# Performance work log

Hardware: AMD Instinct MI355X
Metric: run time of the kernel (lower is better)

## Reference

```python
import jax, jax.numpy as jnp
import numpy as np


def setup_inputs() -> dict:
    key = jax.random.key(0)
    k1, k2 = jax.random.split(key)
    B, D, H, W = 4, 64, 64, 64
    M = 4096
    z = jax.random.normal(k1, (B, D, H, W), dtype=jnp.float32)
    e = jax.random.normal(k2, (M, D), dtype=jnp.float32)
    log_sigma = jnp.zeros((1,), dtype=jnp.float32)
    return {"z": z, "e": e, "log_sigma": log_sigma}


def reference(z, e, log_sigma):
    # z: [B, D, H, W] latents, e: [M, D] codebook, log_sigma: [1] parameter
    T = 1.0  # latent_temp default
    B, D, H, W = z.shape
    zf = jnp.transpose(z, (0, 2, 3, 1)).reshape(-1, D)  # [N, D]
    N = zf.shape[0]
    # squared pairwise distances via ||z||^2 + ||e||^2 - 2 z e^T (avoids [N,M,D] intermediate)
    d2 = (jnp.sum(zf * zf, axis=1)[:, None]
          + jnp.sum(e * e, axis=1)[None, :]
          - 2.0 * zf @ e.T)  # [N, M]
    alpha = -1.0 / (2.0 * jnp.exp(log_sigma[0]) ** 2)
    matrix = alpha * d2 / T  # [N, M]
    lse = jax.nn.logsumexp(matrix, axis=0)  # [M], reduce over N points per code
    # np.log(np.e) == 1.0
    loss = (-jnp.mean(T * lse)
            + 0.5 * D * (2.0 * log_sigma[0] - 1.0)
            + jnp.log(jnp.asarray(N, dtype=jnp.float32)))
    return loss
```

## Files before the change

kernel.cpp:

```cpp
#include <hip/hip_runtime.h>
#include <hip/hip_bf16.h>
#include <math.h>

#define D_   64
#define HW_  4096
#define N_   16384
#define M_   4096

#define BM 128
#define NSPLIT 32
#define NCHUNK (N_ / NSPLIT)
#define NTILES (NCHUNK / 128)

#define AZN_OFF 0
#define AEN_OFF 16384
#define SUM_OFF 20480
#define ZTB_OFF 24576
#define EBF_OFF (24576 + 524288)
#define FAST_WS_FLOATS (EBF_OFF + 131072)

#define FB_AZN 0
#define FB_AEN N_
#define FB_PART (N_ + M_)

#define L2E 1.4426950408889634f

typedef __attribute__((ext_vector_type(8))) short short8;
typedef __attribute__((ext_vector_type(16))) float floatx16;

#if __has_builtin(__builtin_amdgcn_exp2f)
#define EXP2F(x) __builtin_amdgcn_exp2f(x)
#else
#define EXP2F(x) exp2f(x)
#endif

__device__ __forceinline__ unsigned int bf16_rne(float x) {
    unsigned int u = __float_as_uint(x);
    u += 0x7fffu + ((u >> 16) & 1u);
    return u >> 16;
}


__global__ void prep_kernel(const float* __restrict__ z,
                            const float* __restrict__ e,
                            const float* __restrict__ lsp,
                            float* __restrict__ ws) {
    const float ls = lsp[0];
    const float alpha = -0.5f * __expf(-2.f * ls);
    const float anl = alpha * L2E;
    const float c2p = -2.f * alpha * L2E;
    unsigned short* zTb = (unsigned short*)(ws + ZTB_OFF);
    unsigned short* ebf = (unsigned short*)(ws + EBF_OFF);
    const int blk = blockIdx.x, t = threadIdx.x;

    if (blk < 256) {
        __shared__ float lt[64 * 65];
        const int b = blk >> 6, hw0 = (blk & 63) * 64;
        const int n0 = b * HW_ + hw0;
        const float* zb = z + ((size_t)b * D_) * HW_ + hw0;
#pragma unroll
        for (int i = 0; i < 4; ++i) {
            int idx = t + 256 * i;
            int d = idx >> 4, c = (idx & 15) * 4;
            float4 v = *(const float4*)(zb + (size_t)d * HW_ + c);
            float* p = &lt[d * 65 + c];
            p[0] = v.x; p[1] = v.y; p[2] = v.z; p[3] = v.w;
        }
        __syncthreads();
#pragma unroll
        for (int j = 0; j < 2; ++j) {
            int idx = t + 256 * j;
            int nl = idx >> 3, g = idx & 7;
            float v[8]; float s = 0.f;
#pragma unroll
            for (int jj = 0; jj < 8; ++jj) {
                v[jj] = lt[(8 * g + jj) * 65 + nl];
                s = fmaf(v[jj], v[jj], s);
            }
            s += __shfl_xor(s, 1);
            s += __shfl_xor(s, 2);
            s += __shfl_xor(s, 4);
            uint4 pk;
            pk.x = bf16_rne(v[0] * c2p) | (bf16_rne(v[1] * c2p) << 16);
            pk.y = bf16_rne(v[2] * c2p) | (bf16_rne(v[3] * c2p) << 16);
            pk.z = bf16_rne(v[4] * c2p) | (bf16_rne(v[5] * c2p) << 16);
            pk.w = bf16_rne(v[6] * c2p) | (bf16_rne(v[7] * c2p) << 16);
            *(uint4*)(zTb + (size_t)(n0 + nl) * 64 + 8 * g) = pk;
            if (g == 0) ws[AZN_OFF + n0 + nl] = anl * s;
        }
    } else {
        int m = (blk - 256) * 256 + t;
        const float4* ep = (const float4*)(e + (size_t)m * D_);
        float s = 0.f;
        unsigned int pk[32];
#pragma unroll
        for (int k = 0; k < 16; ++k) {
            float4 v = ep[k];
            s += v.x * v.x + v.y * v.y + v.z * v.z + v.w * v.w;
            pk[2 * k]     = bf16_rne(v.x) | (bf16_rne(v.y) << 16);
            pk[2 * k + 1] = bf16_rne(v.z) | (bf16_rne(v.w) << 16);
        }
        uint4* op = (uint4*)(ebf + (size_t)m * 64);
#pragma unroll
        for (int k = 0; k < 8; ++k)
            op[k] = make_uint4(pk[4 * k], pk[4 * k + 1], pk[4 * k + 2], pk[4 * k + 3]);
        ws[AEN_OFF + m] = anl * s;
        ws[SUM_OFF + m] = 0.f;
    }
}

__global__ __launch_bounds__(256, 2) void main_fast(float* __restrict__ ws) {
    __shared__ float lds_red[BM];
    const unsigned short* zTb = (const unsigned short*)(ws + ZTB_OFF);
    const unsigned short* ebf = (const unsigned short*)(ws + EBF_OFF);
    const float* azn = ws + AZN_OFF;
    const float* aen = ws + AEN_OFF;
    float* sums = ws + SUM_OFF;

    const int m0 = blockIdx.x * BM;
    const int ns = blockIdx.y;
    const int t = threadIdx.x;
    const int lane = t & 63;
    const int w = t >> 6;
    const int rlo = lane & 31;
    const int kh = lane >> 5;

    short8 bf[4][4];
    float aen_r[4];
#pragma unroll
    for (int mt = 0; mt < 4; ++mt) {
        int row = m0 + mt * 32 + rlo;
        aen_r[mt] = aen[row];
#pragma unroll
        for (int ks = 0; ks < 4; ++ks)
            bf[mt][ks] = *(const short8*)(ebf + (size_t)row * 64 + (ks * 2 + kh) * 8);
    }

    float sum[4] = {0.f, 0.f, 0.f, 0.f};
    const int nbase = ns * NCHUNK + w * 32;

#pragma unroll
    for (int tile = 0; tile < NTILES; ++tile) {
        const int nr = nbase + tile * 128;
        short8 af[4];
#pragma unroll
        for (int ks = 0; ks < 4; ++ks)
            af[ks] = *(const short8*)(zTb + (size_t)(nr + rlo) * 64 + (ks * 2 + kh) * 8);

        float azn_r[16];
        const int r0 = nr + 4 * kh;
#pragma unroll
        for (int rg = 0; rg < 4; ++rg) {
            float4 vv = *(const float4*)(azn + r0 + 8 * rg);
            azn_r[rg * 4 + 0] = vv.x; azn_r[rg * 4 + 1] = vv.y;
            azn_r[rg * 4 + 2] = vv.z; azn_r[rg * 4 + 3] = vv.w;
        }

        floatx16 acc[4];
#pragma unroll
        for (int mt = 0; mt < 4; ++mt)
#pragma unroll
            for (int r = 0; r < 16; ++r)
                acc[mt][r] = azn_r[r] + aen_r[mt];

#pragma unroll
        for (int ks = 0; ks < 4; ++ks)
#pragma unroll
            for (int mt = 0; mt < 4; ++mt)
                acc[mt] = __builtin_amdgcn_mfma_f32_32x32x16_bf16(
                    af[ks], bf[mt][ks], acc[mt], 0, 0, 0);

#pragma unroll
        for (int mt = 0; mt < 4; ++mt) {
            float s = 0.f;
#pragma unroll
            for (int r = 0; r < 16; ++r) s += EXP2F(acc[mt][r]);
            sum[mt] += s;
        }
    }

#pragma unroll
    for (int mt = 0; mt < 4; ++mt) sum[mt] += __shfl_down(sum[mt], 32);

    if (t < BM) lds_red[t] = 0.f;
    __syncthreads();
    if (lane < 32) {
#pragma unroll
        for (int mt = 0; mt < 4; ++mt) atomicAdd(&lds_red[mt * 32 + rlo], sum[mt]);
    }
    __syncthreads();
    if (t < BM) atomicAdd(&sums[m0 + t], lds_red[t]);
}

__global__ void finalize_fast(const float* __restrict__ ws,
                              const float* __restrict__ lsp,
                              float* __restrict__ out) {
    __shared__ double red[256];
    const float* sums = ws + SUM_OFF;
    int t = threadIdx.x;
    double local = 0.0;
#pragma unroll
    for (int j = 0; j < 16; ++j) {
        float s = sums[t + 256 * j];
        local += (double)logf(s);
    }
    red[t] = local;
    __syncthreads();
    for (int off = 128; off > 0; off >>= 1) {
        if (t < off) red[t] += red[t + off];
        __syncthreads();
    }
    if (t == 0) {
        double ls = (double)lsp[0];
        double loss = -(red[0] / (double)M_)
                      + 0.5 * (double)D_ * (2.0 * ls - 1.0)
                      + log((double)N_);
        out[0] = (float)loss;
    }
}


__global__ void norms_kernel(const float* __restrict__ z,
                             const float* __restrict__ e,
                             const float* __restrict__ lsp,
                             float* __restrict__ ws) {
    float ls = lsp[0];
    float alpha = -0.5f * __expf(-2.f * ls);
    int blk = blockIdx.x, t = threadIdx.x;
    if (blk < 64) {
        int n = blk * 256 + t;
        int b = n >> 12, hw = n & 4095;
        const float* zp = z + (size_t)b * D_ * HW_ + hw;
        float s = 0.f;
#pragma unroll
        for (int d = 0; d < D_; ++d) { float v = zp[(size_t)d * HW_]; s = fmaf(v, v, s); }
        ws[FB_AZN + n] = alpha * s;
    } else {
        int m = (blk - 64) * 256 + t;
        const float4* ep = (const float4*)(e + (size_t)m * D_);
        float s = 0.f;
#pragma unroll
        for (int k = 0; k < 16; ++k) {
            float4 v = ep[k];
            s += v.x * v.x + v.y * v.y + v.z * v.z + v.w * v.w;
        }
        ws[FB_AEN + m] = alpha * s;
    }
}

__global__ __launch_bounds__(256, 2) void main_lds(
        const float* __restrict__ z, const float* __restrict__ e,
        const float* __restrict__ lsp, const float* __restrict__ ws,
        float* __restrict__ partial) {
    __shared__ unsigned short lds_a[128 * 64];
    __shared__ unsigned short lds_b[BM * 64];
    __shared__ float lds_azn[128];
    __shared__ float lds_red[BM];

    const int m0 = blockIdx.x * BM;
    const int ns = blockIdx.y;
    const int t = threadIdx.x;
    const int lane = t & 63;
    const int w = t >> 6;
    const int rlo = lane & 31;
    const int kh = lane >> 5;

    const float ls = lsp[0];
    const float c2 = __expf(-2.f * ls);

    const float* azn_g = ws + FB_AZN;
    const float* aen_g = ws + FB_AEN;

#pragma unroll
    for (int i = 0; i < 8; ++i) {
        int idx = t + 256 * i;
        int m = idx >> 4, f4 = idx & 15;
        float4 v = *(const float4*)(e + (size_t)(m0 + m) * D_ + f4 * 4);
        unsigned int p0 = bf16_rne(v.x) | (bf16_rne(v.y) << 16);
        unsigned int p1 = bf16_rne(v.z) | (bf16_rne(v.w) << 16);
        int un = m * 8 + ((f4 >> 1) ^ (m & 7));
        unsigned int* dst = (unsigned int*)&lds_b[un * 8 + (f4 & 1) * 4];
        dst[0] = p0; dst[1] = p1;
    }
    float aen_r[4];
#pragma unroll
    for (int mt = 0; mt < 4; ++mt) aen_r[mt] = aen_g[m0 + mt * 32 + rlo];
    __syncthreads();

    short8 bfr[4][4];
#pragma unroll
    for (int mt = 0; mt < 4; ++mt)
#pragma unroll
        for (int ks = 0; ks < 4; ++ks) {
            int row = mt * 32 + rlo;
            int g = ks * 2 + kh;
            bfr[mt][ks] = *(const short8*)&lds_b[(row * 8 + (g ^ (row & 7))) * 8];
        }

    float sum[4] = {0.f, 0.f, 0.f, 0.f};

    for (int tile = 0; tile < NTILES; ++tile) {
        int n0 = ns * NCHUNK + tile * 128;
        int b   = n0 >> 12;
        int hw0 = n0 & 4095;
        __syncthreads();
#pragma unroll
        for (int i = 0; i < 4; ++i) {
            int idx = t + 256 * i;
            int dp = idx >> 5;
            int c4 = idx & 31;
            int d0 = dp * 2;
            const float* zp = z + ((size_t)(b * D_ + d0)) * HW_ + hw0 + c4 * 4;
            float4 v0 = *(const float4*)zp;
            float4 v1 = *(const float4*)(zp + HW_);
            int g = d0 >> 3;
            float a0[4] = {v0.x, v0.y, v0.z, v0.w};
            float a1[4] = {v1.x, v1.y, v1.z, v1.w};
#pragma unroll
            for (int q = 0; q < 4; ++q) {
                int row = c4 * 4 + q;
                unsigned int pk = bf16_rne(a0[q]) | (bf16_rne(a1[q]) << 16);
                int un = row * 8 + (g ^ (row & 7));
                *(unsigned int*)&lds_a[un * 8 + (d0 & 7)] = pk;
            }
        }
        if (t < 128) lds_azn[t] = azn_g[n0 + t];
        __syncthreads();

        short8 af[4];
        int arow = w * 32 + rlo;
#pragma unroll
        for (int ks = 0; ks < 4; ++ks) {
            int g = ks * 2 + kh;
            af[ks] = *(const short8*)&lds_a[(arow * 8 + (g ^ (arow & 7))) * 8];
        }
        float azn_r[16];
        int r0 = w * 32 + 4 * kh;
#pragma unroll
        for (int rg = 0; rg < 4; ++rg) {
            float4 vv = *(const float4*)&lds_azn[r0 + 8 * rg];
            azn_r[rg * 4 + 0] = vv.x; azn_r[rg * 4 + 1] = vv.y;
            azn_r[rg * 4 + 2] = vv.z; azn_r[rg * 4 + 3] = vv.w;
        }

        floatx16 acc[4] = {};
#pragma unroll
        for (int ks = 0; ks < 4; ++ks)
#pragma unroll
            for (int mt = 0; mt < 4; ++mt)
                acc[mt] = __builtin_amdgcn_mfma_f32_32x32x16_bf16(
                    af[ks], bfr[mt][ks], acc[mt], 0, 0, 0);

#pragma unroll
        for (int mt = 0; mt < 4; ++mt) {
            float s = 0.f;
#pragma unroll
            for (int r = 0; r < 16; ++r) {
                float val = fmaf(acc[mt][r], c2, azn_r[r]) + aen_r[mt];
                s += __expf(val);
            }
            sum[mt] += s;
        }
    }

#pragma unroll
    for (int mt = 0; mt < 4; ++mt) sum[mt] += __shfl_down(sum[mt], 32);

    __syncthreads();
    if (t < BM) lds_red[t] = 0.f;
    __syncthreads();
    if (lane < 32) {
#pragma unroll
        for (int mt = 0; mt < 4; ++mt) atomicAdd(&lds_red[mt * 32 + rlo], sum[mt]);
    }
    __syncthreads();
    if (t < BM) partial[(size_t)ns * M_ + m0 + t] = lds_red[t];
}

__global__ void finalize_part(const float* __restrict__ partial,
                              const float* __restrict__ lsp,
                              float* __restrict__ out) {
    __shared__ double red[256];
    int t = threadIdx.x;
    double local = 0.0;
#pragma unroll
    for (int j = 0; j < 16; ++j) {
        int m = t + 256 * j;
        float s = 0.f;
#pragma unroll
        for (int k = 0; k < NSPLIT; ++k) s += partial[(size_t)k * M_ + m];
        local += (double)logf(s);
    }
    red[t] = local;
    __syncthreads();
    for (int off = 128; off > 0; off >>= 1) {
        if (t < off) red[t] += red[t + off];
        __syncthreads();
    }
    if (t == 0) {
        double ls = (double)lsp[0];
        double loss = -(red[0] / (double)M_)
                      + 0.5 * (double)D_ * (2.0 * ls - 1.0)
                      + log((double)N_);
        out[0] = (float)loss;
    }
}

extern "C" void kernel_launch(void* const* d_in, const int* in_sizes, int n_in,
                              void* d_out, int out_size, void* d_ws, size_t ws_size,
                              hipStream_t stream) {
    const float* z   = (const float*)d_in[0];
    const float* e   = (const float*)d_in[1];
    const float* lsp = (const float*)d_in[2];
    float* ws  = (float*)d_ws;
    float* out = (float*)d_out;

    if (ws_size >= (size_t)FAST_WS_FLOATS * sizeof(float)) {
        hipLaunchKernelGGL(prep_kernel, dim3(272), dim3(256), 0, stream, z, e, lsp, ws);
        hipLaunchKernelGGL(main_fast, dim3(M_ / BM, NSPLIT), dim3(256), 0, stream, ws);
        hipLaunchKernelGGL(finalize_fast, dim3(1), dim3(256), 0, stream, ws, lsp, out);
    } else {
        hipLaunchKernelGGL(norms_kernel, dim3(80), dim3(256), 0, stream, z, e, lsp, ws);
        hipLaunchKernelGGL(main_lds, dim3(M_ / BM, NSPLIT), dim3(256), 0, stream,
                           z, e, lsp, ws, ws + FB_PART);
        hipLaunchKernelGGL(finalize_part, dim3(1), dim3(256), 0, stream,
                           ws + FB_PART, lsp, out);
    }
}
```

Measured before the change: 86.47 us.

## Shrink codebook tile, lengthen N chunks, and prefetch next z tile in registers

Each main_fast block now covers 64 codes instead of 128 and splits N into 16 chunks instead of 32, so every block runs 8 N-tiles rather than 4. The z fragment and its norms for the next tile are loaded into registers while the current tile computes, a software double buffer meant to hide global load latency. Occupancy is raised to 3 waves per SIMD. The grid stays at 1024 blocks but each block does half the MFMA work per tile and reloads z twice as often relative to compute. The fallback path is hardcoded to its old sizes so it keeps working.

New measurement: 91.41 us. 1.06x slower.

```diff
diff --git a/kernel.cpp b/kernel.cpp
--- a/kernel.cpp
+++ b/kernel.cpp
@@ -7,8 +7,8 @@
 #define N_   16384
 #define M_   4096
 
-#define BM 128
-#define NSPLIT 32
+#define BM 64
+#define NSPLIT 16
 #define NCHUNK (N_ / NSPLIT)
 #define NTILES (NCHUNK / 128)
 
@@ -109,7 +109,7 @@
     }
 }
 
-__global__ __launch_bounds__(256, 2) void main_fast(float* __restrict__ ws) {
+__global__ __launch_bounds__(256, 3) void main_fast(float* __restrict__ ws) {
     __shared__ float lds_red[BM];
     const unsigned short* zTb = (const unsigned short*)(ws + ZTB_OFF);
     const unsigned short* ebf = (const unsigned short*)(ws + EBF_OFF);
@@ -125,10 +125,10 @@
     const int rlo = lane & 31;
     const int kh = lane >> 5;
 
-    short8 bf[4][4];
-    float aen_r[4];
-#pragma unroll
-    for (int mt = 0; mt < 4; ++mt) {
+    short8 bf[2][4];
+    float aen_r[2];
+#pragma unroll
+    for (int mt = 0; mt < 2; ++mt) {
         int row = m0 + mt * 32 + rlo;
         aen_r[mt] = aen[row];
 #pragma unroll
@@ -136,29 +136,45 @@
             bf[mt][ks] = *(const short8*)(ebf + (size_t)row * 64 + (ks * 2 + kh) * 8);
     }
 
-    float sum[4] = {0.f, 0.f, 0.f, 0.f};
+    float sum[2] = {0.f, 0.f};
     const int nbase = ns * NCHUNK + w * 32;
 
+    short8 afc[4];
+    float4 aznc[4];
+    {
+        const int nr = nbase;
+#pragma unroll
+        for (int ks = 0; ks < 4; ++ks)
+            afc[ks] = *(const short8*)(zTb + (size_t)(nr + rlo) * 64 + (ks * 2 + kh) * 8);
+        const int r0 = nr + 4 * kh;
+#pragma unroll
+        for (int rg = 0; rg < 4; ++rg) aznc[rg] = *(const float4*)(azn + r0 + 8 * rg);
+    }
+
 #pragma unroll
     for (int tile = 0; tile < NTILES; ++tile) {
-        const int nr = nbase + tile * 128;
-        short8 af[4];
-#pragma unroll
-        for (int ks = 0; ks < 4; ++ks)
-            af[ks] = *(const short8*)(zTb + (size_t)(nr + rlo) * 64 + (ks * 2 + kh) * 8);
+        short8 afn[4];
+        float4 aznn[4];
+        if (tile + 1 < NTILES) {
+            const int nr = nbase + (tile + 1) * 128;
+#pragma unroll
+            for (int ks = 0; ks < 4; ++ks)
+                afn[ks] = *(const short8*)(zTb + (size_t)(nr + rlo) * 64 + (ks * 2 + kh) * 8);
+            const int r0 = nr + 4 * kh;
+#pragma unroll
+            for (int rg = 0; rg < 4; ++rg) aznn[rg] = *(const float4*)(azn + r0 + 8 * rg);
+        }
 
         float azn_r[16];
-        const int r0 = nr + 4 * kh;
 #pragma unroll
         for (int rg = 0; rg < 4; ++rg) {
-            float4 vv = *(const float4*)(azn + r0 + 8 * rg);
-            azn_r[rg * 4 + 0] = vv.x; azn_r[rg * 4 + 1] = vv.y;
-            azn_r[rg * 4 + 2] = vv.z; azn_r[rg * 4 + 3] = vv.w;
-        }
-
-        floatx16 acc[4];
-#pragma unroll
-        for (int mt = 0; mt < 4; ++mt)
+            azn_r[rg * 4 + 0] = aznc[rg].x; azn_r[rg * 4 + 1] = aznc[rg].y;
+            azn_r[rg * 4 + 2] = aznc[rg].z; azn_r[rg * 4 + 3] = aznc[rg].w;
+        }
+
+        floatx16 acc[2];
+#pragma unroll
+        for (int mt = 0; mt < 2; ++mt)
 #pragma unroll
             for (int r = 0; r < 16; ++r)
                 acc[mt][r] = azn_r[r] + aen_r[mt];
@@ -166,27 +182,32 @@
 #pragma unroll
         for (int ks = 0; ks < 4; ++ks)
 #pragma unroll
-            for (int mt = 0; mt < 4; ++mt)
+            for (int mt = 0; mt < 2; ++mt)
                 acc[mt] = __builtin_amdgcn_mfma_f32_32x32x16_bf16(
-                    af[ks], bf[mt][ks], acc[mt], 0, 0, 0);
-
-#pragma unroll
-        for (int mt = 0; mt < 4; ++mt) {
+                    afc[ks], bf[mt][ks], acc[mt], 0, 0, 0);
+
+#pragma unroll
+        for (int mt = 0; mt < 2; ++mt) {
             float s = 0.f;
 #pragma unroll
             for (int r = 0; r < 16; ++r) s += EXP2F(acc[mt][r]);
             sum[mt] += s;
         }
-    }
-
-#pragma unroll
-    for (int mt = 0; mt < 4; ++mt) sum[mt] += __shfl_down(sum[mt], 32);
+
+#pragma unroll
+        for (int ks = 0; ks < 4; ++ks) afc[ks] = afn[ks];
+#pragma unroll
+        for (int rg = 0; rg < 4; ++rg) aznc[rg] = aznn[rg];
+    }
+
+#pragma unroll
+    for (int mt = 0; mt < 2; ++mt) sum[mt] += __shfl_down(sum[mt], 32);
 
     if (t < BM) lds_red[t] = 0.f;
     __syncthreads();
     if (lane < 32) {
 #pragma unroll
-        for (int mt = 0; mt < 4; ++mt) atomicAdd(&lds_red[mt * 32 + rlo], sum[mt]);
+        for (int mt = 0; mt < 2; ++mt) atomicAdd(&lds_red[mt * 32 + rlo], sum[mt]);
     }
     __syncthreads();
     if (t < BM) atomicAdd(&sums[m0 + t], lds_red[t]);
@@ -253,11 +274,11 @@
         const float* __restrict__ lsp, const float* __restrict__ ws,
         float* __restrict__ partial) {
     __shared__ unsigned short lds_a[128 * 64];
-    __shared__ unsigned short lds_b[BM * 64];
+    __shared__ unsigned short lds_b[128 * 64];
     __shared__ float lds_azn[128];
-    __shared__ float lds_red[BM];
-
-    const int m0 = blockIdx.x * BM;
+    __shared__ float lds_red[128];
+
+    const int m0 = blockIdx.x * 128;
     const int ns = blockIdx.y;
     const int t = threadIdx.x;
     const int lane = t & 63;
@@ -299,8 +320,8 @@
 
     float sum[4] = {0.f, 0.f, 0.f, 0.f};
 
-    for (int tile = 0; tile < NTILES; ++tile) {
-        int n0 = ns * NCHUNK + tile * 128;
+    for (int tile = 0; tile < 4; ++tile) {
+        int n0 = ns * 512 + tile * 128;
         int b   = n0 >> 12;
         int hw0 = n0 & 4095;
         __syncthreads();
@@ -367,14 +388,14 @@
     for (int mt = 0; mt < 4; ++mt) sum[mt] += __shfl_down(sum[mt], 32);
 
     __syncthreads();
-    if (t < BM) lds_red[t] = 0.f;
+    if (t < 128) lds_red[t] = 0.f;
     __syncthreads();
     if (lane < 32) {
 #pragma unroll
         for (int mt = 0; mt < 4; ++mt) atomicAdd(&lds_red[mt * 32 + rlo], sum[mt]);
     }
     __syncthreads();
-    if (t < BM) partial[(size_t)ns * M_ + m0 + t] = lds_red[t];
+    if (t < 128) partial[(size_t)ns * M_ + m0 + t] = lds_red[t];
 }
 
 __global__ void finalize_part(const float* __restrict__ partial,
@@ -388,7 +409,7 @@
         int m = t + 256 * j;
         float s = 0.f;
 #pragma unroll
-        for (int k = 0; k < NSPLIT; ++k) s += partial[(size_t)k * M_ + m];
+        for (int k = 0; k < 32; ++k) s += partial[(size_t)k * M_ + m];
         local += (double)logf(s);
     }
     red[t] = local;
@@ -421,7 +442,7 @@
         hipLaunchKernelGGL(finalize_fast, dim3(1), dim3(256), 0, stream, ws, lsp, out);
     } else {
         hipLaunchKernelGGL(norms_kernel, dim3(80), dim3(256), 0, stream, z, e, lsp, ws);
-        hipLaunchKernelGGL(main_lds, dim3(M_ / BM, NSPLIT), dim3(256), 0, stream,
+        hipLaunchKernelGGL(main_lds, dim3(32, 32), dim3(256), 0, stream,
                            z, e, lsp, ws, ws + FB_PART);
         hipLaunchKernelGGL(finalize_part, dim3(1), dim3(256), 0, stream,
                            ws + FB_PART, lsp, out);
```
